# Kernel tuning notes

Hardware: AMD Instinct MI355X
Metric: run time of the kernel (lower is better)

The kernel has to match this reference:

```python
import jax, jax.numpy as jnp
import numpy as np

B, T, D_IN, H = 256, 512, 512, 1024
LN_EPS = 1e-5


def setup_inputs() -> dict:
    key = jax.random.key(0)
    ks = jax.random.split(key, 12)

    def xavier(k, shape):
        fan_in, fan_out = shape[1], shape[0]
        lim = np.sqrt(6.0 / (fan_in + fan_out))
        return jax.random.uniform(k, shape, jnp.float32, -lim, lim)

    # PyTorch GRUCell default init: U(-1/sqrt(H), 1/sqrt(H))
    s = 1.0 / np.sqrt(H)
    return {
        "inputs": jax.random.normal(ks[0], (B, T, D_IN), jnp.float32),
        "mask": jax.random.uniform(ks[1], (B, T), jnp.float32),
        "cond_bias_in": jax.random.normal(ks[2], (B, H), jnp.float32),
        "cond_bias_gate": jax.random.normal(ks[3], (B, H), jnp.float32),
        "W_in": xavier(ks[4], (H, D_IN)),
        "b_in": jnp.zeros((H,), jnp.float32),
        "W_gate": xavier(ks[5], (H, D_IN)),
        "b_gate": jnp.zeros((H,), jnp.float32),
        "W_ih": jax.random.uniform(ks[6], (3 * H, H), jnp.float32, -s, s),
        "b_ih": jax.random.uniform(ks[7], (3 * H,), jnp.float32, -s, s),
        "W_hh": jax.random.uniform(ks[8], (3 * H, H), jnp.float32, -s, s),
        "b_hh": jax.random.uniform(ks[9], (3 * H,), jnp.float32, -s, s),
        "ln_g": jnp.ones((H,), jnp.float32),
        "ln_b": jnp.zeros((H,), jnp.float32),
    }


def reference(inputs, mask, cond_bias_in, cond_bias_gate,
              W_in, b_in, W_gate, b_gate,
              W_ih, b_ih, W_hh, b_hh, ln_g, ln_b):
    # gated input projection: tanh(in_proj(x)+cb_in) * sigmoid(gate_proj(x)+cb_gate)
    x_lin = jnp.einsum('btd,hd->bth', inputs, W_in) + b_in + cond_bias_in[:, None, :]
    g_lin = jnp.einsum('btd,hd->bth', inputs, W_gate) + b_gate + cond_bias_gate[:, None, :]
    x = jnp.tanh(x_lin) * jax.nn.sigmoid(g_lin)  # [B,T,H]

    # precompute input-side GRU gates for all timesteps (one big GEMM)
    gi_all = jnp.einsum('bth,gh->btg', x, W_ih) + b_ih  # [B,T,3H]
    gi_all = jnp.swapaxes(gi_all, 0, 1)                  # [T,B,3H]
    m_all = jnp.swapaxes(mask, 0, 1)[:, :, None]         # [T,B,1]

    hdim = W_hh.shape[1]

    def step(h, inp):
        gi, mt = inp
        gh = h @ W_hh.T + b_hh  # [B,3H]
        i_r, i_z, i_n = gi[:, :hdim], gi[:, hdim:2 * hdim], gi[:, 2 * hdim:]
        h_r, h_z, h_n = gh[:, :hdim], gh[:, hdim:2 * hdim], gh[:, 2 * hdim:]
        r = jax.nn.sigmoid(i_r + h_r)
        z = jax.nn.sigmoid(i_z + h_z)
        n = jnp.tanh(i_n + r * h_n)
        new_h = (1.0 - z) * n + z * h
        h = jnp.where(mt > 0.5, new_h, h)
        return h, h

    h0 = jnp.zeros((x.shape[0], hdim), x.dtype)
    _, ys = jax.lax.scan(step, h0, (gi_all, m_all))  # ys: [T,B,H]
    y = jnp.swapaxes(ys, 0, 1)                        # [B,T,H]

    # LayerNorm over last dim
    mu = jnp.mean(y, axis=-1, keepdims=True)
    var = jnp.mean(jnp.square(y - mu), axis=-1, keepdims=True)
    y = (y - mu) * jax.lax.rsqrt(var + LN_EPS) * ln_g + ln_b
    return y
```

## Files before the change

### kernel.cpp

```cpp
#include <hip/hip_runtime.h>
#include <stdint.h>

#define B_ 256
#define T_ 512
#define DIN 512
#define H_ 1024
#define BT (B_*T_)
#define G3 (3*H_)
#define RS 100

typedef unsigned short u16;
typedef unsigned int u32;
typedef unsigned long long u64;
typedef __attribute__((ext_vector_type(8))) __bf16 bf16x8;
typedef __attribute__((ext_vector_type(4))) float f4;

__device__ __forceinline__ u16 f2bf(float f){
  u32 u = __float_as_uint(f);
  u32 r = u + 0x7fffu + ((u>>16)&1u);
  return (u16)(r>>16);
}
__device__ __forceinline__ float bf2f(u16 u){ return __uint_as_float(((u32)u)<<16); }
__device__ __forceinline__ float sigm(float x){ return 1.f/(1.f+__expf(-x)); }
__device__ __forceinline__ float tanh_f(float x){
  x = fminf(fmaxf(x, -15.f), 15.f);
  float e = __expf(2.f*x);
  return (e-1.f)/(e+1.f);
}
__device__ __forceinline__ void gload_lds16(const u16* g, u16* l){
  __builtin_amdgcn_global_load_lds((const __attribute__((address_space(1))) void*)g,
                                   (__attribute__((address_space(3))) void*)l, 16, 0, 0);
}
__device__ __forceinline__ f4 mfma16(bf16x8 a, bf16x8 b, f4 c){
  return __builtin_amdgcn_mfma_f32_16x16x32_bf16(a, b, c, 0, 0, 0);
}

__global__ __launch_bounds__(256) void k_cast(const float* __restrict__ s,
                                              u16* __restrict__ d, int n8){
  int i = blockIdx.x*256 + threadIdx.x;
  int st = gridDim.x*256;
  for (; i < n8; i += st){
    float4 a = ((const float4*)s)[i*2+0];
    float4 b = ((const float4*)s)[i*2+1];
    uint4 o;
    o.x = (u32)f2bf(a.x) | ((u32)f2bf(a.y)<<16);
    o.y = (u32)f2bf(a.z) | ((u32)f2bf(a.w)<<16);
    o.z = (u32)f2bf(b.x) | ((u32)f2bf(b.y)<<16);
    o.w = (u32)f2bf(b.z) | ((u32)f2bf(b.w)<<16);
    ((uint4*)d)[i] = o;
  }
}

__global__ __launch_bounds__(256) void k_prep(const float* __restrict__ mask,
                                              u16* __restrict__ act, u16* __restrict__ idx,
                                              int* __restrict__ nact, int* __restrict__ meta){
  int b = blockIdx.x, tid = threadIdx.x;
  __shared__ int ps[256];
  const float* mr = mask + (size_t)b*T_;
  int a0 = (mr[2*tid]   > 0.5f) ? 1 : 0;
  int a1 = (mr[2*tid+1] > 0.5f) ? 1 : 0;
  ps[tid] = a0 + a1;
  __syncthreads();
  for (int off=1; off<256; off<<=1){
    int v = ps[tid];
    int u = (tid >= off) ? ps[tid-off] : 0;
    __syncthreads();
    ps[tid] = v + u;
    __syncthreads();
  }
  int excl = tid ? ps[tid-1] : 0;
  int i0 = excl + a0;
  int i1 = i0 + a1;
  idx[b*T_ + 2*tid]   = (u16)i0;
  idx[b*T_ + 2*tid+1] = (u16)i1;
  if (a0) act[b*T_ + i0-1] = (u16)(2*tid);
  if (a1) act[b*T_ + i1-1] = (u16)(2*tid+1);
  int na = ps[255];
  if (tid == 0){
    nact[b] = na;
    atomicMax(&meta[0], na);
    atomicMax(&meta[1 + (b>>5)], na);
  }
  for (int s = na + tid; s < T_; s += 256) act[b*T_ + s] = (u16)(T_-1);
}

__global__ __launch_bounds__(256) void k_phase1c(
    const u16* __restrict__ A, const u16* __restrict__ Wi, const u16* __restrict__ Wg,
    const u16* __restrict__ act, const int* __restrict__ meta,
    const float* __restrict__ bin, const float* __restrict__ bgt,
    const float* __restrict__ cbi, const float* __restrict__ cbg,
    u16* __restrict__ X){
  __shared__ u16 As[128*32];
  __shared__ u16 Bi[64*32];
  __shared__ u16 Bg[64*32];
  int tid = threadIdx.x;
  int lane = tid & 63, wave = tid >> 6;
  int l15 = lane & 15, l4 = lane >> 4;
  int blk = blockIdx.x;
  int chunk = blk >> 7;
  int wi = blk & 127;
  int m0 = (chunk*8 + (wi & 7))*128;
  int n0 = (wi >> 3)*64;
  if (m0 >= (meta[0] << 8)) return;
  int mo = (wave&1)*64, no = (wave>>1)*32;

  int r0 = m0 + (tid>>2), r1 = r0 + 64;
  int b0r = r0 & 255, s0r = r0 >> 8;
  int b1r = r1 & 255, s1r = r1 >> 8;
  const u16* a0p = A + ((size_t)b0r*T_ + act[b0r*T_ + s0r])*DIN + (tid&3)*8;
  const u16* a1p = A + ((size_t)b1r*T_ + act[b1r*T_ + s1r])*DIN + (tid&3)*8;

  f4 acc1[4][2] = {}; f4 acc2[4][2] = {};
  for (int k0 = 0; k0 < DIN; k0 += 32){
    gload_lds16(a0p + k0, As + wave*512);
    gload_lds16(a1p + k0, As + (4+wave)*512);
    int u = tid;
    gload_lds16(Wi + (n0 + (u>>2))*DIN + k0 + (u&3)*8, Bi + wave*512);
    gload_lds16(Wg + (n0 + (u>>2))*DIN + k0 + (u&3)*8, Bg + wave*512);
    __syncthreads();
    bf16x8 a[4], b1[2], b2[2];
    #pragma unroll
    for (int mt=0; mt<4; mt++) a[mt] = *(const bf16x8*)&As[(mo+mt*16+l15)*32 + l4*8];
    #pragma unroll
    for (int nt=0; nt<2; nt++){
      b1[nt] = *(const bf16x8*)&Bi[(no+nt*16+l15)*32 + l4*8];
      b2[nt] = *(const bf16x8*)&Bg[(no+nt*16+l15)*32 + l4*8];
    }
    #pragma unroll
    for (int mt=0; mt<4; mt++)
      #pragma unroll
      for (int nt=0; nt<2; nt++){
        acc1[mt][nt] = mfma16(a[mt], b1[nt], acc1[mt][nt]);
        acc2[mt][nt] = mfma16(a[mt], b2[nt], acc2[mt][nt]);
      }
    __syncthreads();
  }
  #pragma unroll
  for (int mt=0; mt<4; mt++)
   #pragma unroll
   for (int nt=0; nt<2; nt++)
    #pragma unroll
    for (int i=0; i<4; i++){
      int m = m0 + mo + mt*16 + l4*4 + i;
      int n = n0 + no + nt*16 + l15;
      int b = m & 255;
      float xl = acc1[mt][nt][i] + bin[n] + cbi[b*H_ + n];
      float gl = acc2[mt][nt][i] + bgt[n] + cbg[b*H_ + n];
      X[(size_t)m*H_ + n] = f2bf(tanh_f(xl) * sigm(gl));
    }
}

__global__ __launch_bounds__(256) void k_phase2c(
    const u16* __restrict__ X, const u16* __restrict__ W,
    const int* __restrict__ meta, const float* __restrict__ bih,
    u16* __restrict__ GI){
  __shared__ u16 As[128*32];
  __shared__ u16 Bs[128*32];
  int tid = threadIdx.x;
  int lane = tid & 63, wave = tid >> 6;
  int l15 = lane & 15, l4 = lane >> 4;
  int blk = blockIdx.x;
  int chunk = 255 - (blk / 96);
  int wi = blk % 96;
  int m0 = (chunk*4 + (wi & 3))*128;
  int n0 = (wi >> 2)*128;
  if (m0 >= (meta[0] << 8)) return;
  int mo = (wave&1)*64, no = (wave>>1)*64;
  f4 acc[4][4] = {};
  for (int k0 = 0; k0 < H_; k0 += 32){
    int u = tid;
    gload_lds16(X + (m0 + (u>>2))*H_ + k0 + (u&3)*8, As + wave*512);
    gload_lds16(W + (n0 + (u>>2))*H_ + k0 + (u&3)*8, Bs + wave*512);
    u = 256 + tid;
    gload_lds16(X + (m0 + (u>>2))*H_ + k0 + (u&3)*8, As + (4+wave)*512);
    gload_lds16(W + (n0 + (u>>2))*H_ + k0 + (u&3)*8, Bs + (4+wave)*512);
    __syncthreads();
    bf16x8 a[4], b[4];
    #pragma unroll
    for (int t2=0; t2<4; t2++){
      a[t2] = *(const bf16x8*)&As[(mo+t2*16+l15)*32 + l4*8];
      b[t2] = *(const bf16x8*)&Bs[(no+t2*16+l15)*32 + l4*8];
    }
    #pragma unroll
    for (int mt=0; mt<4; mt++)
      #pragma unroll
      for (int nt=0; nt<4; nt++)
        acc[mt][nt] = mfma16(a[mt], b[nt], acc[mt][nt]);
    __syncthreads();
  }
  #pragma unroll
  for (int mt=0; mt<4; mt++)
   #pragma unroll
   for (int nt=0; nt<4; nt++)
    #pragma unroll
    for (int i=0; i<4; i++){
      int m = m0 + mo + mt*16 + l4*4 + i;
      int n = n0 + no + nt*16 + l15;
      GI[(size_t)m*G3 + n] = f2bf(acc[mt][nt][i] + bih[n]);
    }
}

__global__ __launch_bounds__(256,1) void k_scan_c(
    const u16* __restrict__ GI, const u16* __restrict__ Whh,
    const float* __restrict__ bhh,
    const int* __restrict__ nact, const int* __restrict__ meta,
    u16* __restrict__ hcomp, int* __restrict__ flags){
  __shared__ u16 hs[32*1024];
  __shared__ float red[2*32*RS];
  int tid = threadIdx.x;
  int lane = tid & 63, wave = tid >> 6;
  int l15 = lane & 15, l4 = lane >> 4;
  int bi = blockIdx.x & 7, ji = blockIdx.x >> 3;
  int b0 = bi*32, j0 = ji*32;
  int kwi = wave & 1;
  int kw2 = kwi*512;
  int nw  = (wave>>1)*48;

  f4 wff[3][16];
  #pragma unroll
  for (int nt=0; nt<3; nt++){
    int c  = nw + nt*16 + l15;
    int wrow = (c>>5)*H_ + j0 + (c&31);
    #pragma unroll
    for (int ks=0; ks<16; ks++){
      wff[nt][ks] = *(const f4*)&Whh[(size_t)wrow*H_ + kw2 + ks*32 + l4*8];
      asm volatile("" : "+v"(wff[nt][ks]));
    }
  }

  int urow = tid >> 3;
  int c0 = (tid & 7)*4;
  int row_b = b0 + urow;
  float bh[3][4];
  #pragma unroll
  for (int g=0; g<3; g++)
    #pragma unroll
    for (int ci=0; ci<4; ci++)
      bh[g][ci] = bhh[g*H_ + j0 + c0 + ci];
  float hreg[4] = {0.f,0.f,0.f,0.f};
  int na = nact[row_b];
  int Smax = meta[1 + bi];

  u64 gv0 = 0, gv1 = 0, gv2 = 0;
  if (Smax > 0){
    const u16* gib0 = GI + ((size_t)row_b)*G3 + j0 + c0;
    gv0 = *(const u64*)(gib0);
    gv1 = *(const u64*)(gib0 + H_);
    gv2 = *(const u64*)(gib0 + 2*H_);
  }

  for (int s=0; s<Smax; s++){
    if (wave == 0 && s > 0){
      const int* fp = flags + (bi*32 + (lane & 31))*4;
      u32 it = 0;
      for (;;){
        int f = __hip_atomic_load(fp, __ATOMIC_RELAXED, __HIP_MEMORY_SCOPE_AGENT);
        if (__all(f >= s)) break;
        __builtin_amdgcn_s_sleep(1);
        if (++it > 300000u) break;
      }
    }
    __syncthreads();

    if (s == 0){
      uint4 z = {0,0,0,0};
      uint4* hs4 = (uint4*)hs;
      #pragma unroll
      for (int i=0; i<16; i++) hs4[i*256 + tid] = z;
    } else {
      const uint4* hb4 = (const uint4*)(hcomp + (size_t)(s-1)*(B_*H_) + (size_t)b0*H_);
      uint4 r[16];
      #pragma unroll
      for (int i=0; i<16; i++){
        const uint4* p = hb4 + i*256 + tid;
        asm volatile("global_load_dwordx4 %0, %1, off" : "=v"(r[i]) : "v"(p));
      }
      asm volatile("s_waitcnt vmcnt(0)" ::: "memory");
      __builtin_amdgcn_sched_barrier(0);
      uint4* hs4 = (uint4*)hs;
      #pragma unroll
      for (int i=0; i<16; i++){
        int g = i*256 + tid;
        int row = g >> 7, col = g & 127;
        hs4[row*128 + (col ^ (row&7))] = r[i];
      }
    }
    __syncthreads();

    u64 nv0 = gv0, nv1 = gv1, nv2 = gv2;
    if (s+1 < Smax){
      const u16* gibn = GI + ((size_t)(s+1)*B_ + row_b)*G3 + j0 + c0;
      nv0 = *(const u64*)(gibn);
      nv1 = *(const u64*)(gibn + H_);
      nv2 = *(const u64*)(gibn + 2*H_);
    }

    f4 acc[2][3] = {};
    #pragma unroll
    for (int ks=0; ks<16; ks++){
      bf16x8 a[2];
      #pragma unroll
      for (int mt=0; mt<2; mt++){
        int row = mt*16 + l15;
        int c16 = (kw2>>3) + ks*4 + l4;
        a[mt] = *(const bf16x8*)&hs[row*1024 + ((c16 ^ (row&7))<<3)];
      }
      #pragma unroll
      for (int mt=0; mt<2; mt++)
        #pragma unroll
        for (int nt=0; nt<3; nt++)
          acc[mt][nt] = mfma16(a[mt], __builtin_bit_cast(bf16x8, wff[nt][ks]), acc[mt][nt]);
    }

    #pragma unroll
    for (int mt=0; mt<2; mt++)
      #pragma unroll
      for (int nt=0; nt<3; nt++)
        #pragma unroll
        for (int i=0; i<4; i++)
          red[(kwi*32 + mt*16 + l4*4 + i)*RS + nw + nt*16 + l15] = acc[mt][nt][i];
    __syncthreads();

    {
      f4 gh[3];
      #pragma unroll
      for (int g=0; g<3; g++){
        f4 s0 = *(const f4*)&red[(0*32+urow)*RS + g*32 + c0];
        f4 s1 = *(const f4*)&red[(1*32+urow)*RS + g*32 + c0];
        gh[g] = s0 + s1;
      }
      bool active = (s < na);
      u16 hb16[4];
      #pragma unroll
      for (int ci=0; ci<4; ci++){
        float ir  = bf2f((u16)(gv0 >> (16*ci)));
        float iz  = bf2f((u16)(gv1 >> (16*ci)));
        float in_ = bf2f((u16)(gv2 >> (16*ci)));
        float r = sigm(ir + gh[0][ci] + bh[0][ci]);
        float z = sigm(iz + gh[1][ci] + bh[1][ci]);
        float n = tanh_f(in_ + r*(gh[2][ci] + bh[2][ci]));
        float hn = (1.f - z)*n + z*hreg[ci];
        hreg[ci] = active ? hn : hreg[ci];
        hb16[ci] = f2bf(hreg[ci]);
      }
      u64 pk = (u64)hb16[0] | ((u64)hb16[1]<<16) | ((u64)hb16[2]<<32) | ((u64)hb16[3]<<48);
      __hip_atomic_store((u64*)&hcomp[(size_t)s*(B_*H_) + (size_t)row_b*H_ + j0 + c0],
                         pk, __ATOMIC_RELAXED, __HIP_MEMORY_SCOPE_AGENT);
    }
    __syncthreads();
    if (tid == 0)
      __hip_atomic_store(&flags[(bi*32 + ji)*4], s+1,
                         __ATOMIC_RELEASE, __HIP_MEMORY_SCOPE_AGENT);
    gv0 = nv0; gv1 = nv1; gv2 = nv2;
  }
}

__global__ __launch_bounds__(256) void k_lng8(const u16* __restrict__ hcomp,
                                              const u16* __restrict__ idx,
                                              const float* __restrict__ g,
                                              const float* __restrict__ b,
                                              float* __restrict__ Y){
  int blk = blockIdx.x;
  int bb = blk >> 6, tt0 = (blk & 63)*8;
  int tid = threadIdx.x;
  float4 gg = ((const float4*)g)[tid];
  float4 bb4 = ((const float4*)b)[tid];
  __shared__ float ss[4], qq[4];
  int wave = tid >> 6;
  #pragma unroll
  for (int rr=0; rr<8; rr++){
    int tt = tt0 + rr;
    int s = (int)idx[bb*T_ + tt];
    float4 v;
    if (s == 0){
      v.x = v.y = v.z = v.w = 0.f;
    } else {
      u64 hv = *(const u64*)(hcomp + (size_t)(s-1)*(B_*H_) + (size_t)bb*H_ + tid*4);
      v.x = bf2f((u16)hv);
      v.y = bf2f((u16)(hv>>16));
      v.z = bf2f((u16)(hv>>32));
      v.w = bf2f((u16)(hv>>48));
    }
    float sm = v.x+v.y+v.z+v.w;
    float q = v.x*v.x+v.y*v.y+v.z*v.z+v.w*v.w;
    #pragma unroll
    for (int off=32; off; off>>=1){ sm += __shfl_down(sm, off); q += __shfl_down(q, off); }
    if ((tid&63)==0){ ss[wave]=sm; qq[wave]=q; }
    __syncthreads();
    sm = ss[0]+ss[1]+ss[2]+ss[3];
    q  = qq[0]+qq[1]+qq[2]+qq[3];
    float mu = sm*(1.f/H_);
    float var = q*(1.f/H_) - mu*mu;
    float rs = rsqrtf(var + 1e-5f);
    float4 o;
    o.x = (v.x-mu)*rs*gg.x + bb4.x;
    o.y = (v.y-mu)*rs*gg.y + bb4.y;
    o.z = (v.z-mu)*rs*gg.z + bb4.z;
    o.w = (v.w-mu)*rs*gg.w + bb4.w;
    ((float4*)(Y + ((size_t)bb*T_ + tt)*H_))[tid] = o;
    __syncthreads();
  }
}

__global__ __launch_bounds__(256) void k_phase1(
    const u16* __restrict__ A, const u16* __restrict__ Wi, const u16* __restrict__ Wg,
    const float* __restrict__ bin, const float* __restrict__ bgt,
    const float* __restrict__ cbi, const float* __restrict__ cbg,
    u16* __restrict__ X){
  __shared__ u16 As[128*32];
  __shared__ u16 Bi[64*32];
  __shared__ u16 Bg[64*32];
  int tid = threadIdx.x;
  int lane = tid & 63, wave = tid >> 6;
  int l15 = lane & 15, l4 = lane >> 4;
  int blk = blockIdx.x;
  int chunk = blk >> 7;
  int wi = blk & 127;
  int m0 = (chunk*8 + (wi & 7))*128;
  int n0 = (wi >> 3)*64;
  int mo = (wave&1)*64, no = (wave>>1)*32;
  f4 acc1[4][2] = {}; f4 acc2[4][2] = {};
  for (int k0 = 0; k0 < DIN; k0 += 32){
    int u = tid;
    gload_lds16(A + (m0 + (u>>2))*DIN + k0 + (u&3)*8, As + wave*512);
    u = 256 + tid;
    gload_lds16(A + (m0 + (u>>2))*DIN + k0 + (u&3)*8, As + (4+wave)*512);
    u = tid;
    gload_lds16(Wi + (n0 + (u>>2))*DIN + k0 + (u&3)*8, Bi + wave*512);
    gload_lds16(Wg + (n0 + (u>>2))*DIN + k0 + (u&3)*8, Bg + wave*512);
    __syncthreads();
    bf16x8 a[4], b1[2], b2[2];
    #pragma unroll
    for (int mt=0; mt<4; mt++) a[mt] = *(const bf16x8*)&As[(mo+mt*16+l15)*32 + l4*8];
    #pragma unroll
    for (int nt=0; nt<2; nt++){
      b1[nt] = *(const bf16x8*)&Bi[(no+nt*16+l15)*32 + l4*8];
      b2[nt] = *(const bf16x8*)&Bg[(no+nt*16+l15)*32 + l4*8];
    }
    #pragma unroll
    for (int mt=0; mt<4; mt++)
      #pragma unroll
      for (int nt=0; nt<2; nt++){
        acc1[mt][nt] = mfma16(a[mt], b1[nt], acc1[mt][nt]);
        acc2[mt][nt] = mfma16(a[mt], b2[nt], acc2[mt][nt]);
      }
    __syncthreads();
  }
  #pragma unroll
  for (int mt=0; mt<4; mt++)
   #pragma unroll
   for (int nt=0; nt<2; nt++)
    #pragma unroll
    for (int i=0; i<4; i++){
      int m = m0 + mo + mt*16 + l4*4 + i;
      int n = n0 + no + nt*16 + l15;
      int b = m >> 9;
      float xl = acc1[mt][nt][i] + bin[n] + cbi[b*H_ + n];
      float gl = acc2[mt][nt][i] + bgt[n] + cbg[b*H_ + n];
      X[(size_t)m*H_ + n] = f2bf(tanh_f(xl) * sigm(gl));
    }
}

__global__ __launch_bounds__(256) void k_phase2(
    const u16* __restrict__ X, const u16* __restrict__ W,
    const float* __restrict__ bih, u16* __restrict__ GI){
  __shared__ u16 As[128*32];
  __shared__ u16 Bs[128*32];
  int tid = threadIdx.x;
  int lane = tid & 63, wave = tid >> 6;
  int l15 = lane & 15, l4 = lane >> 4;
  int blk = blockIdx.x;
  int chunk = blk / 96;
  int wi = blk % 96;
  int m0 = (chunk*4 + (wi & 3))*128;
  int n0 = (wi >> 2)*128;
  int mo = (wave&1)*64, no = (wave>>1)*64;
  f4 acc[4][4] = {};
  for (int k0 = 0; k0 < H_; k0 += 32){
    int u = tid;
    gload_lds16(X + (m0 + (u>>2))*H_ + k0 + (u&3)*8, As + wave*512);
    gload_lds16(W + (n0 + (u>>2))*H_ + k0 + (u&3)*8, Bs + wave*512);
    u = 256 + tid;
    gload_lds16(X + (m0 + (u>>2))*H_ + k0 + (u&3)*8, As + (4+wave)*512);
    gload_lds16(W + (n0 + (u>>2))*H_ + k0 + (u&3)*8, Bs + (4+wave)*512);
    __syncthreads();
    bf16x8 a[4], b[4];
    #pragma unroll
    for (int t2=0; t2<4; t2++){
      a[t2] = *(const bf16x8*)&As[(mo+t2*16+l15)*32 + l4*8];
      b[t2] = *(const bf16x8*)&Bs[(no+t2*16+l15)*32 + l4*8];
    }
    #pragma unroll
    for (int mt=0; mt<4; mt++)
      #pragma unroll
      for (int nt=0; nt<4; nt++)
        acc[mt][nt] = mfma16(a[mt], b[nt], acc[mt][nt]);
    __syncthreads();
  }
  #pragma unroll
  for (int mt=0; mt<4; mt++)
   #pragma unroll
   for (int nt=0; nt<4; nt++)
    #pragma unroll
    for (int i=0; i<4; i++){
      int m = m0 + mo + mt*16 + l4*4 + i;
      int n = n0 + no + nt*16 + l15;
      int b = m >> 9, t = m & 511;
      GI[((size_t)t*B_ + b)*G3 + n] = f2bf(acc[mt][nt][i] + bih[n]);
    }
}

__global__ __launch_bounds__(256,1) void k_scan_d(
    const u16* __restrict__ GI, const u16* __restrict__ Whh,
    const float* __restrict__ bhh, const float* __restrict__ mask,
    u16* __restrict__ hbuf, int* __restrict__ flags, float* __restrict__ Y){
  __shared__ u16 hs[32*1024];
  __shared__ float red[2*32*RS];
  int tid = threadIdx.x;
  int lane = tid & 63, wave = tid >> 6;
  int l15 = lane & 15, l4 = lane >> 4;
  int bi = blockIdx.x & 7, ji = blockIdx.x >> 3;
  int b0 = bi*32, j0 = ji*32;
  int kwi = wave & 1;
  int kw2 = kwi*512;
  int nw  = (wave>>1)*48;
  f4 wff[3][16];
  #pragma unroll
  for (int nt=0; nt<3; nt++){
    int c  = nw + nt*16 + l15;
    int wrow = (c>>5)*H_ + j0 + (c&31);
    #pragma unroll
    for (int ks=0; ks<16; ks++){
      wff[nt][ks] = *(const f4*)&Whh[(size_t)wrow*H_ + kw2 + ks*32 + l4*8];
      asm volatile("" : "+v"(wff[nt][ks]));
    }
  }
  int urow = tid >> 3;
  int c0 = (tid & 7)*4;
  float bh[3][4];
  #pragma unroll
  for (int g=0; g<3; g++)
    #pragma unroll
    for (int ci=0; ci<4; ci++)
      bh[g][ci] = bhh[g*H_ + j0 + c0 + ci];
  float hreg[4] = {0.f,0.f,0.f,0.f};
  const float* mrow = mask + (size_t)(b0+urow)*T_;
  u64* hs64 = (u64*)hs;
  for (int t=0; t<T_; t++){
    const u16* gib = GI + ((size_t)t*B_ + (b0+urow))*G3 + j0 + c0;
    u64 gv0 = *(const u64*)(gib);
    u64 gv1 = *(const u64*)(gib + H_);
    u64 gv2 = *(const u64*)(gib + 2*H_);
    float msk = mrow[t];
    if (wave == 0 && t > 0){
      const int* fp = flags + (bi*32 + (lane & 31))*4;
      u32 it = 0;
      for (;;){
        int f = __hip_atomic_load(fp, __ATOMIC_RELAXED, __HIP_MEMORY_SCOPE_AGENT);
        if (__all(f >= t)) break;
        __builtin_amdgcn_s_sleep(1);
        if (++it > 300000u) break;
      }
    }
    __syncthreads();
    {
      const u64* hb = (const u64*)hbuf + (size_t)(t&1)*(B_*H_/4) + (size_t)b0*256;
      #pragma unroll
      for (int ib=0; ib<4; ib++){
        u64 v[8];
        #pragma unroll
        for (int i=0; i<8; i++)
          v[i] = __hip_atomic_load(hb + (ib*8+i)*256 + tid,
                                   __ATOMIC_RELAXED, __HIP_MEMORY_SCOPE_AGENT);
        #pragma unroll
        for (int i=0; i<8; i++){
          int row = ib*8 + i;
          int phys = (((tid>>1) ^ (row&7))<<1) | (tid&1);
          hs64[row*256 + phys] = v[i];
        }
      }
    }
    __syncthreads();
    f4 acc[2][3] = {};
    #pragma unroll
    for (int ks=0; ks<16; ks++){
      bf16x8 a[2];
      #pragma unroll
      for (int mt=0; mt<2; mt++){
        int row = mt*16 + l15;
        int c16 = (kw2>>3) + ks*4 + l4;
        a[mt] = *(const bf16x8*)&hs[row*1024 + ((c16 ^ (row&7))<<3)];
      }
      #pragma unroll
      for (int mt=0; mt<2; mt++)
        #pragma unroll
        for (int nt=0; nt<3; nt++)
          acc[mt][nt] = mfma16(a[mt], __builtin_bit_cast(bf16x8, wff[nt][ks]), acc[mt][nt]);
    }
    #pragma unroll
    for (int mt=0; mt<2; mt++)
      #pragma unroll
      for (int nt=0; nt<3; nt++)
        #pragma unroll
        for (int i=0; i<4; i++)
          red[(kwi*32 + mt*16 + l4*4 + i)*RS + nw + nt*16 + l15] = acc[mt][nt][i];
    __syncthreads();
    {
      f4 gh[3];
      #pragma unroll
      for (int g=0; g<3; g++){
        f4 s0 = *(const f4*)&red[(0*32+urow)*RS + g*32 + c0];
        f4 s1 = *(const f4*)&red[(1*32+urow)*RS + g*32 + c0];
        gh[g] = s0 + s1;
      }
      u16 hb16[4];
      float yv[4];
      #pragma unroll
      for (int ci=0; ci<4; ci++){
        float ir  = bf2f((u16)(gv0 >> (16*ci)));
        float iz  = bf2f((u16)(gv1 >> (16*ci)));
        float in_ = bf2f((u16)(gv2 >> (16*ci)));
        float r = sigm(ir + gh[0][ci] + bh[0][ci]);
        float z = sigm(iz + gh[1][ci] + bh[1][ci]);
        float n = tanh_f(in_ + r*(gh[2][ci] + bh[2][ci]));
        float hn = (1.f - z)*n + z*hreg[ci];
        hreg[ci] = (msk > 0.5f) ? hn : hreg[ci];
        hb16[ci] = f2bf(hreg[ci]);
        yv[ci] = hreg[ci];
      }
      u64 pk = (u64)hb16[0] | ((u64)hb16[1]<<16) | ((u64)hb16[2]<<32) | ((u64)hb16[3]<<48);
      __hip_atomic_store((u64*)&hbuf[(size_t)((t+1)&1)*(B_*H_) + (size_t)(b0+urow)*H_ + j0 + c0],
                         pk, __ATOMIC_RELAXED, __HIP_MEMORY_SCOPE_AGENT);
      float4 yq; yq.x=yv[0]; yq.y=yv[1]; yq.z=yv[2]; yq.w=yv[3];
      *(float4*)&Y[((size_t)(b0+urow)*T_ + t)*H_ + j0 + c0] = yq;
    }
    __syncthreads();
    if (tid == 0)
      __hip_atomic_store(&flags[(bi*32 + ji)*4], t+1,
                         __ATOMIC_RELEASE, __HIP_MEMORY_SCOPE_AGENT);
  }
}

__global__ __launch_bounds__(256) void k_ln(float* __restrict__ Y,
                                            const float* __restrict__ g,
                                            const float* __restrict__ b){
  int row = blockIdx.x, tid = threadIdx.x;
  float4 v = ((const float4*)(Y + (size_t)row*H_))[tid];
  float s = v.x+v.y+v.z+v.w;
  float q = v.x*v.x+v.y*v.y+v.z*v.z+v.w*v.w;
  #pragma unroll
  for (int off=32; off; off>>=1){ s += __shfl_down(s, off); q += __shfl_down(q, off); }
  __shared__ float ss[4], qq[4];
  int wave = tid >> 6;
  if ((tid&63)==0){ ss[wave]=s; qq[wave]=q; }
  __syncthreads();
  s = ss[0]+ss[1]+ss[2]+ss[3];
  q = qq[0]+qq[1]+qq[2]+qq[3];
  float mu = s*(1.f/H_);
  float var = q*(1.f/H_) - mu*mu;
  float rs = rsqrtf(var + 1e-5f);
  float4 gg = ((const float4*)g)[tid];
  float4 bb = ((const float4*)b)[tid];
  float4 o;
  o.x = (v.x-mu)*rs*gg.x + bb.x;
  o.y = (v.y-mu)*rs*gg.y + bb.y;
  o.z = (v.z-mu)*rs*gg.z + bb.z;
  o.w = (v.w-mu)*rs*gg.w + bb.w;
  ((float4*)(Y + (size_t)row*H_))[tid] = o;
}

extern "C" void kernel_launch(void* const* d_in, const int* in_sizes, int n_in,
                              void* d_out, int out_size, void* d_ws, size_t ws_size,
                              hipStream_t stream){
  const float* inputs = (const float*)d_in[0];
  const float* mask   = (const float*)d_in[1];
  const float* cbi    = (const float*)d_in[2];
  const float* cbg    = (const float*)d_in[3];
  const float* W_in   = (const float*)d_in[4];
  const float* b_in   = (const float*)d_in[5];
  const float* W_gate = (const float*)d_in[6];
  const float* b_gate = (const float*)d_in[7];
  const float* W_ih   = (const float*)d_in[8];
  const float* b_ih   = (const float*)d_in[9];
  const float* W_hh   = (const float*)d_in[10];
  const float* b_hh   = (const float*)d_in[11];
  const float* ln_g   = (const float*)d_in[12];
  const float* ln_b   = (const float*)d_in[13];

  char* ws = (char*)d_ws;
  size_t o = 0;
  u16* in_bf  = (u16*)(ws + o); o += (size_t)BT*DIN*2;
  u16* wi_bf  = (u16*)(ws + o); o += (size_t)H_*DIN*2;
  u16* wg_bf  = (u16*)(ws + o); o += (size_t)H_*DIN*2;
  u16* wih_bf = (u16*)(ws + o); o += (size_t)G3*H_*2;
  u16* whh_bf = (u16*)(ws + o); o += (size_t)G3*H_*2;
  u16* gi_bf  = (u16*)(ws + o); o += (size_t)T_*B_*G3*2;
  u16* actb   = (u16*)(ws + o); o += (size_t)B_*T_*2;
  u16* idxb   = (u16*)(ws + o); o += (size_t)B_*T_*2;
  int* nactb  = (int*)(ws + o); o += (size_t)B_*4;
  int* meta   = (int*)(ws + o); o += 256;
  int* flags  = (int*)(ws + o); o += (size_t)8*32*4*4;
  u16* hbuf   = (u16*)(ws + o); o += (size_t)2*B_*H_*2;
  size_t need_direct = o;
  u16* hcomp  = (u16*)(ws + o); o += (size_t)T_*B_*H_*2;
  size_t need_comp = o;
  if (ws_size < need_direct) return;
  bool comp = (ws_size >= need_comp);

  hipMemsetAsync(flags, 0, (size_t)8*32*4*4, stream);
  if (comp) hipMemsetAsync(meta, 0, 256, stream);
  else      hipMemsetAsync(hbuf, 0, (size_t)2*B_*H_*2, stream);

  k_cast<<<2048,256,0,stream>>>(inputs, in_bf, BT*DIN/8);
  k_cast<<<256, 256,0,stream>>>(W_in,   wi_bf,  H_*DIN/8);
  k_cast<<<256, 256,0,stream>>>(W_gate, wg_bf,  H_*DIN/8);
  k_cast<<<1024,256,0,stream>>>(W_ih,   wih_bf, G3*H_/8);
  k_cast<<<1024,256,0,stream>>>(W_hh,   whh_bf, G3*H_/8);

  u16* X = (u16*)d_out;

  if (comp){
    k_prep<<<B_,256,0,stream>>>(mask, actb, idxb, nactb, meta);
    k_phase1c<<<16384,256,0,stream>>>(in_bf, wi_bf, wg_bf, actb, meta,
                                      b_in, b_gate, cbi, cbg, X);
    k_phase2c<<<24576,256,0,stream>>>(X, wih_bf, meta, b_ih, gi_bf);
    k_scan_c<<<256,256,0,stream>>>(gi_bf, whh_bf, b_hh, nactb, meta, hcomp, flags);
    k_lng8<<<BT/8,256,0,stream>>>(hcomp, idxb, ln_g, ln_b, (float*)d_out);
  } else {
    k_phase1<<<16384,256,0,stream>>>(in_bf, wi_bf, wg_bf, b_in, b_gate, cbi, cbg, X);
    k_phase2<<<24576,256,0,stream>>>(X, wih_bf, b_ih, gi_bf);
    k_scan_d<<<256,256,0,stream>>>(gi_bf, whh_bf, b_hh, mask, hbuf, flags, (float*)d_out);
    k_ln<<<BT,256,0,stream>>>((float*)d_out, ln_g, ln_b);
  }
}
```

Baseline: 3.175 ms.

## Split recurrent scan into 16-row batch groups with two blocks per CU

The persistent GRU scan kernel now gives each block 16 batch rows instead of 32 and launches 512 blocks, two resident per CU. Each block's per-step work halves: hidden-state tile loads, MFMAs and gate math. The per-group max step count is now computed over 16 rows. The aim is to shorten the serial per-step critical path and use more of the machine. The costs are twice as many flag-synchronised blocks, higher register pressure from sharing a CU, and weight fragments held redundantly across twice as many blocks.

New measurement: 3.655 ms. 15.1% more time.

```diff
diff --git a/kernel.cpp b/kernel.cpp
--- a/kernel.cpp
+++ b/kernel.cpp
@@ -14,6 +14,7 @@
 typedef unsigned long long u64;
 typedef __attribute__((ext_vector_type(8))) __bf16 bf16x8;
 typedef __attribute__((ext_vector_type(4))) float f4;
+typedef __attribute__((ext_vector_type(2))) float f2;
 
 __device__ __forceinline__ u16 f2bf(float f){
   u32 u = __float_as_uint(f);
@@ -79,7 +80,7 @@
   if (tid == 0){
     nact[b] = na;
     atomicMax(&meta[0], na);
-    atomicMax(&meta[1 + (b>>5)], na);
+    atomicMax(&meta[1 + (b>>4)], na);
   }
   for (int s = na + tid; s < T_; s += 256) act[b*T_ + s] = (u16)(T_-1);
 }
@@ -200,18 +201,18 @@
     }
 }
 
-__global__ __launch_bounds__(256,1) void k_scan_c(
+__global__ __launch_bounds__(256,2) void k_scan_c(
     const u16* __restrict__ GI, const u16* __restrict__ Whh,
     const float* __restrict__ bhh,
     const int* __restrict__ nact, const int* __restrict__ meta,
     u16* __restrict__ hcomp, int* __restrict__ flags){
-  __shared__ u16 hs[32*1024];
-  __shared__ float red[2*32*RS];
+  __shared__ u16 hs[16*1024];
+  __shared__ float red[2*16*RS];
   int tid = threadIdx.x;
   int lane = tid & 63, wave = tid >> 6;
   int l15 = lane & 15, l4 = lane >> 4;
-  int bi = blockIdx.x & 7, ji = blockIdx.x >> 3;
-  int b0 = bi*32, j0 = ji*32;
+  int bi = blockIdx.x & 15, ji = blockIdx.x >> 4;
+  int b0 = bi*16, j0 = ji*32;
   int kwi = wave & 1;
   int kw2 = kwi*512;
   int nw  = (wave>>1)*48;
@@ -228,25 +229,25 @@
     }
   }
 
-  int urow = tid >> 3;
-  int c0 = (tid & 7)*4;
+  int urow = tid >> 4;
+  int c0 = (tid & 15)*2;
   int row_b = b0 + urow;
-  float bh[3][4];
-  #pragma unroll
-  for (int g=0; g<3; g++)
-    #pragma unroll
-    for (int ci=0; ci<4; ci++)
-      bh[g][ci] = bhh[g*H_ + j0 + c0 + ci];
-  float hreg[4] = {0.f,0.f,0.f,0.f};
+  float bh[3][2];
+  #pragma unroll
+  for (int g=0; g<3; g++){
+    bh[g][0] = bhh[g*H_ + j0 + c0];
+    bh[g][1] = bhh[g*H_ + j0 + c0 + 1];
+  }
+  float hreg[2] = {0.f, 0.f};
   int na = nact[row_b];
   int Smax = meta[1 + bi];
 
-  u64 gv0 = 0, gv1 = 0, gv2 = 0;
+  u32 gv0 = 0, gv1 = 0, gv2 = 0;
   if (Smax > 0){
     const u16* gib0 = GI + ((size_t)row_b)*G3 + j0 + c0;
-    gv0 = *(const u64*)(gib0);
-    gv1 = *(const u64*)(gib0 + H_);
-    gv2 = *(const u64*)(gib0 + 2*H_);
+    gv0 = *(const u32*)(gib0);
+    gv1 = *(const u32*)(gib0 + H_);
+    gv2 = *(const u32*)(gib0 + 2*H_);
   }
 
   for (int s=0; s<Smax; s++){
@@ -266,12 +267,12 @@
       uint4 z = {0,0,0,0};
       uint4* hs4 = (uint4*)hs;
       #pragma unroll
-      for (int i=0; i<16; i++) hs4[i*256 + tid] = z;
+      for (int i=0; i<8; i++) hs4[i*256 + tid] = z;
     } else {
       const uint4* hb4 = (const uint4*)(hcomp + (size_t)(s-1)*(B_*H_) + (size_t)b0*H_);
-      uint4 r[16];
-      #pragma unroll
-      for (int i=0; i<16; i++){
+      uint4 r[8];
+      #pragma unroll
+      for (int i=0; i<8; i++){
         const uint4* p = hb4 + i*256 + tid;
         asm volatile("global_load_dwordx4 %0, %1, off" : "=v"(r[i]) : "v"(p));
       }
@@ -279,7 +280,7 @@
       __builtin_amdgcn_sched_barrier(0);
       uint4* hs4 = (uint4*)hs;
       #pragma unroll
-      for (int i=0; i<16; i++){
+      for (int i=0; i<8; i++){
         int g = i*256 + tid;
         int row = g >> 7, col = g & 127;
         hs4[row*128 + (col ^ (row&7))] = r[i];
@@ -287,52 +288,44 @@
     }
     __syncthreads();
 
-    u64 nv0 = gv0, nv1 = gv1, nv2 = gv2;
+    u32 nv0 = gv0, nv1 = gv1, nv2 = gv2;
     if (s+1 < Smax){
       const u16* gibn = GI + ((size_t)(s+1)*B_ + row_b)*G3 + j0 + c0;
-      nv0 = *(const u64*)(gibn);
-      nv1 = *(const u64*)(gibn + H_);
-      nv2 = *(const u64*)(gibn + 2*H_);
-    }
-
-    f4 acc[2][3] = {};
+      nv0 = *(const u32*)(gibn);
+      nv1 = *(const u32*)(gibn + H_);
+      nv2 = *(const u32*)(gibn + 2*H_);
+    }
+
+    f4 acc[3] = {};
     #pragma unroll
     for (int ks=0; ks<16; ks++){
-      bf16x8 a[2];
-      #pragma unroll
-      for (int mt=0; mt<2; mt++){
-        int row = mt*16 + l15;
-        int c16 = (kw2>>3) + ks*4 + l4;
-        a[mt] = *(const bf16x8*)&hs[row*1024 + ((c16 ^ (row&7))<<3)];
-      }
-      #pragma unroll
-      for (int mt=0; mt<2; mt++)
-        #pragma unroll
-        for (int nt=0; nt<3; nt++)
-          acc[mt][nt] = mfma16(a[mt], __builtin_bit_cast(bf16x8, wff[nt][ks]), acc[mt][nt]);
-    }
-
-    #pragma unroll
-    for (int mt=0; mt<2; mt++)
+      int row = l15;
+      int c16 = (kw2>>3) + ks*4 + l4;
+      bf16x8 a = *(const bf16x8*)&hs[row*1024 + ((c16 ^ (row&7))<<3)];
       #pragma unroll
       for (int nt=0; nt<3; nt++)
-        #pragma unroll
-        for (int i=0; i<4; i++)
-          red[(kwi*32 + mt*16 + l4*4 + i)*RS + nw + nt*16 + l15] = acc[mt][nt][i];
+        acc[nt] = mfma16(a, __builtin_bit_cast(bf16x8, wff[nt][ks]), acc[nt]);
+    }
+
+    #pragma unroll
+    for (int nt=0; nt<3; nt++)
+      #pragma unroll
+      for (int i=0; i<4; i++)
+        red[(kwi*16 + l4*4 + i)*RS + nw + nt*16 + l15] = acc[nt][i];
     __syncthreads();
 
     {
-      f4 gh[3];
+      f2 gh[3];
       #pragma unroll
       for (int g=0; g<3; g++){
-        f4 s0 = *(const f4*)&red[(0*32+urow)*RS + g*32 + c0];
-        f4 s1 = *(const f4*)&red[(1*32+urow)*RS + g*32 + c0];
+        f2 s0 = *(const f2*)&red[(0*16+urow)*RS + g*32 + c0];
+        f2 s1 = *(const f2*)&red[(1*16+urow)*RS + g*32 + c0];
         gh[g] = s0 + s1;
       }
       bool active = (s < na);
-      u16 hb16[4];
-      #pragma unroll
-      for (int ci=0; ci<4; ci++){
+      u16 hb16[2];
+      #pragma unroll
+      for (int ci=0; ci<2; ci++){
         float ir  = bf2f((u16)(gv0 >> (16*ci)));
         float iz  = bf2f((u16)(gv1 >> (16*ci)));
         float in_ = bf2f((u16)(gv2 >> (16*ci)));
@@ -343,8 +336,8 @@
         hreg[ci] = active ? hn : hreg[ci];
         hb16[ci] = f2bf(hreg[ci]);
       }
-      u64 pk = (u64)hb16[0] | ((u64)hb16[1]<<16) | ((u64)hb16[2]<<32) | ((u64)hb16[3]<<48);
-      __hip_atomic_store((u64*)&hcomp[(size_t)s*(B_*H_) + (size_t)row_b*H_ + j0 + c0],
+      u32 pk = (u32)hb16[0] | ((u32)hb16[1]<<16);
+      __hip_atomic_store((u32*)&hcomp[(size_t)s*(B_*H_) + (size_t)row_b*H_ + j0 + c0],
                          pk, __ATOMIC_RELAXED, __HIP_MEMORY_SCOPE_AGENT);
     }
     __syncthreads();
@@ -699,7 +692,7 @@
   u16* idxb   = (u16*)(ws + o); o += (size_t)B_*T_*2;
   int* nactb  = (int*)(ws + o); o += (size_t)B_*4;
   int* meta   = (int*)(ws + o); o += 256;
-  int* flags  = (int*)(ws + o); o += (size_t)8*32*4*4;
+  int* flags  = (int*)(ws + o); o += (size_t)16*32*4*4;
   u16* hbuf   = (u16*)(ws + o); o += (size_t)2*B_*H_*2;
   size_t need_direct = o;
   u16* hcomp  = (u16*)(ws + o); o += (size_t)T_*B_*H_*2;
@@ -707,7 +700,7 @@
   if (ws_size < need_direct) return;
   bool comp = (ws_size >= need_comp);
 
-  hipMemsetAsync(flags, 0, (size_t)8*32*4*4, stream);
+  hipMemsetAsync(flags, 0, (size_t)16*32*4*4, stream);
   if (comp) hipMemsetAsync(meta, 0, 256, stream);
   else      hipMemsetAsync(hbuf, 0, (size_t)2*B_*H_*2, stream);
 
@@ -724,7 +717,7 @@
     k_phase1c<<<16384,256,0,stream>>>(in_bf, wi_bf, wg_bf, actb, meta,
                                       b_in, b_gate, cbi, cbg, X);
     k_phase2c<<<24576,256,0,stream>>>(X, wih_bf, meta, b_ih, gi_bf);
-    k_scan_c<<<256,256,0,stream>>>(gi_bf, whh_bf, b_hh, nactb, meta, hcomp, flags);
+    k_scan_c<<<512,256,0,stream>>>(gi_bf, whh_bf, b_hh, nactb, meta, hcomp, flags);
     k_lng8<<<BT/8,256,0,stream>>>(hcomp, idxb, ln_g, ln_b, (float*)d_out);
   } else {
     k_phase1<<<16384,256,0,stream>>>(in_bf, wi_bf, wg_bf, b_in, b_gate, cbi, cbg, X);
```
